# Optimization experiments

Hardware: AMD Instinct MI355X
Metric: run time of the kernel (lower is better)

## Reference

```python
import jax, jax.numpy as jnp
import numpy as np

E = 1024
M = 6
GH = 256
FR = 16  # FiLM bottleneck r = max(16, E//64)


def setup_inputs() -> dict:
    key = jax.random.key(0)
    ks = jax.random.split(key, 32)
    n = lambda k, shape, std=0.02: jax.random.normal(k, shape, dtype=jnp.float32) * std
    inp = {
        "x": jax.random.normal(ks[0], (4, 2048, E), dtype=jnp.float32),
        # gate MLP E->GH->M
        "gw1": n(ks[1], (E, GH)), "gb1": jnp.zeros((GH,), jnp.float32),
        "gw2": n(ks[2], (GH, M)), "gb2": jnp.zeros((M,), jnp.float32),
        "ebias": jnp.zeros((M,), jnp.float32),
        "pm_alpha": jnp.float32(0.5),
        # expert 0: DoubleMLP E->2E->E
        "dfc_w": n(ks[3], (E, 2 * E)), "dfc_b": jnp.zeros((2 * E,), jnp.float32),
        "dproj_w": n(ks[4], (2 * E, E)), "dproj_b": jnp.zeros((E,), jnp.float32),
        # expert 1: SingleMLP E->E->E
        "sfc_w": n(ks[5], (E, E)), "sfc_b": jnp.zeros((E,), jnp.float32),
        "sproj_w": n(ks[6], (E, E)), "sproj_b": jnp.zeros((E,), jnp.float32),
        # expert 2: rank-2 perceptron
        "p2_w": n(ks[7], (2, E)), "p2_v": n(ks[8], (2, E)),
        "p2_alpha": jnp.ones((2,), jnp.float32), "p2_b": jnp.zeros((2,), jnp.float32),
        "p2_bias": jnp.zeros((E,), jnp.float32),
        # expert 3: rank-4 perceptron
        "p4_w": n(ks[9], (4, E)), "p4_v": n(ks[10], (4, E)),
        "p4_alpha": jnp.ones((4,), jnp.float32), "p4_b": jnp.zeros((4,), jnp.float32),
        "p4_bias": jnp.zeros((E,), jnp.float32),
        # expert 4: ReGLU1D
        "rg_u": n(ks[11], (E,)), "rg_a": jnp.ones((E,), jnp.float32),
        "rg_b": jnp.zeros((1,), jnp.float32), "rg_bias": jnp.zeros((E,), jnp.float32),
        # expert 5: FiLM E->FR->2E
        "fl_dw": n(ks[12], (E, FR)), "fl_db": jnp.zeros((FR,), jnp.float32),
        "fl_uw": n(ks[13], (FR, 2 * E)), "fl_ub": jnp.zeros((2 * E,), jnp.float32),
    }
    return inp


def _gelu(x):
    return jax.nn.gelu(x, approximate=False)  # torch nn.GELU default (erf)


def _rank_n(x, w, v, alpha, b, biasvec):
    # y = biasvec + sum_i alpha_i * gelu(<w_i,x> + b_i) * v_i
    s = jnp.einsum("bse,ne->bsn", x, w) + b
    g = _gelu(s)
    return jnp.einsum("bsn,ne->bse", alpha * g, v) + biasvec


def reference(x, gw1, gb1, gw2, gb2, ebias, pm_alpha,
              dfc_w, dfc_b, dproj_w, dproj_b,
              sfc_w, sfc_b, sproj_w, sproj_b,
              p2_w, p2_v, p2_alpha, p2_b, p2_bias,
              p4_w, p4_v, p4_alpha, p4_b, p4_bias,
              rg_u, rg_a, rg_b, rg_bias,
              fl_dw, fl_db, fl_uw, fl_ub):
    # gate logits [B,S,M]; tau=1.0
    gl = _gelu(x @ gw1 + gb1) @ gw2 + gb2 + ebias
    pi = jax.nn.softmax(gl, axis=-1)
    # top_k=1 sparse weights: mask to top-1 then renormalize
    _, topi = jax.lax.top_k(pi, 1)
    mask = jax.nn.one_hot(topi[..., 0], M, dtype=pi.dtype)
    w = pi * mask
    w = w / (jnp.sum(w, axis=-1, keepdims=True) + 1e-9)

    # experts (dropout = identity in eval)
    o0 = _gelu(x @ dfc_w + dfc_b) @ dproj_w + dproj_b            # DoubleMLP
    o1 = _gelu(x @ sfc_w + sfc_b) @ sproj_w + sproj_b            # SingleMLP
    o2 = _rank_n(x, p2_w, p2_v, p2_alpha, p2_b, p2_bias)          # perc2
    o3 = _rank_n(x, p4_w, p4_v, p4_alpha, p4_b, p4_bias)          # perc4
    s = x @ rg_u + rg_b[0]                                        # ReGLU1D
    o4 = jax.nn.sigmoid(s)[..., None] * (x * rg_a) + rg_bias
    t = _gelu(x @ fl_dw + fl_db)                                  # FiLM
    gb = t @ fl_uw + fl_ub
    gamma, beta = jnp.split(gb, 2, axis=-1)
    o5 = gamma * x + beta

    all_out = jnp.stack([o0, o1, o2, o3, o4, o5], axis=-1)        # [B,S,E,M]
    mixed = jnp.sum(all_out * w[..., None, :], axis=-1)
    return pm_alpha * mixed
```

## Files before the change

### kernel.cpp

```cpp
#include <hip/hip_runtime.h>
#include <math.h>


#define E 1024
#define GH 256
#define NEXP 6
#define NTOK 8192

typedef __attribute__((ext_vector_type(8))) short bf16x8;
typedef __attribute__((ext_vector_type(4))) float f32x4;

__device__ __forceinline__ float gelu_erf(float v) {
    return 0.5f * v * (1.0f + erff(v * 0.70710678118654752440f));
}

__device__ __forceinline__ unsigned short f2bf(float f) {
    union { float f; unsigned u; } c; c.f = f;
    unsigned u = c.u;
    u += 0x7fffu + ((u >> 16) & 1u);
    return (unsigned short)(u >> 16);
}

__device__ __forceinline__ float bf2f(unsigned short h) {
    union { unsigned u; float f; } c; c.u = ((unsigned)h) << 16;
    return c.f;
}

__device__ __forceinline__ float dot4(float4 a, float4 b) {
    return a.x * b.x + a.y * b.y + a.z * b.z + a.w * b.w;
}

__device__ __forceinline__ int ldso(int row, int q) {
    return row * 32 + ((q ^ ((row >> 1) & 3)) << 3);
}

__global__ __launch_bounds__(256)
void prep_kernel(const float* __restrict__ x, unsigned short* __restrict__ xh,
                 unsigned short* __restrict__ xl,
                 const float* __restrict__ gw1, unsigned short* __restrict__ w1cat,
                 const float* __restrict__ fl_dw, float* __restrict__ fl_dwT,
                 const float* __restrict__ dfc_w, unsigned short* __restrict__ dfc_wt,
                 const float* __restrict__ dproj_w, unsigned short* __restrict__ dpj_wt,
                 const float* __restrict__ sfc_w, unsigned short* __restrict__ sfc_wt,
                 const float* __restrict__ sproj_w, unsigned short* __restrict__ spj_wt) {
    __shared__ float tile[32][33];
    const int tid = threadIdx.x;
    const int tx = tid & 31, ty = tid >> 5;
    int b = blockIdx.x;
    if (b < 2048) {
        const int n4 = NTOK * E / 4;
        for (int i = b * 256 + tid; i < n4; i += 2048 * 256) {
            float4 v = reinterpret_cast<const float4*>(x)[i];
            ushort4 h, l;
            h.x = f2bf(v.x); l.x = f2bf(v.x - bf2f(h.x));
            h.y = f2bf(v.y); l.y = f2bf(v.y - bf2f(h.y));
            h.z = f2bf(v.z); l.z = f2bf(v.z - bf2f(h.z));
            h.w = f2bf(v.w); l.w = f2bf(v.w - bf2f(h.w));
            reinterpret_cast<ushort4*>(xh)[i] = h;
            reinterpret_cast<ushort4*>(xl)[i] = l;
        }
        return;
    }
    b -= 2048;
    if (b < 256) {
        const int c0 = (b & 7) * 32, r0 = (b >> 3) * 32;
#pragma unroll
        for (int i = 0; i < 4; ++i)
            tile[ty + i * 8][tx] = gw1[(size_t)(r0 + ty + i * 8) * GH + c0 + tx];
        __syncthreads();
#pragma unroll
        for (int i = 0; i < 4; ++i) {
            float v = tile[tx][ty + i * 8];
            unsigned short h = f2bf(v);
            size_t row = (size_t)(c0 + ty + i * 8) * 2048;
            w1cat[row + r0 + tx] = h;
            w1cat[row + 1024 + r0 + tx] = f2bf(v - bf2f(h));
        }
        return;
    }
    b -= 256;
    if (b < 64) {
        int idx = b * 256 + tid;
        int j = idx >> 10, k = idx & (E - 1);
        fl_dwT[idx] = fl_dw[k * 16 + j];
        return;
    }
    b -= 64;
    const float* src; unsigned short* dst; int R, C, nbx;
    if (b < 2048)      { src = dfc_w;   dst = dfc_wt; R = 1024; C = 2048; nbx = 64; }
    else if (b < 4096) { src = dproj_w; dst = dpj_wt; R = 2048; C = 1024; nbx = 32; b -= 2048; }
    else if (b < 5120) { src = sfc_w;   dst = sfc_wt; R = 1024; C = 1024; nbx = 32; b -= 4096; }
    else               { src = sproj_w; dst = spj_wt; R = 1024; C = 1024; nbx = 32; b -= 5120; }
    const int c0 = (b % nbx) * 32, r0 = (b / nbx) * 32;
#pragma unroll
    for (int i = 0; i < 4; ++i)
        tile[ty + i * 8][tx] = src[(size_t)(r0 + ty + i * 8) * C + c0 + tx];
    __syncthreads();
#pragma unroll
    for (int i = 0; i < 4; ++i)
        dst[(size_t)(c0 + ty + i * 8) * R + r0 + tx] = f2bf(tile[tx][ty + i * 8]);
}

__global__ __launch_bounds__(256)
void gate_partial_kernel(const unsigned short* __restrict__ xh,
                         const unsigned short* __restrict__ xl,
                         const unsigned short* __restrict__ w1cat,
                         float* __restrict__ hp0, float* __restrict__ hp1) {
    __shared__ __align__(16) unsigned short As[128 * 32];
    __shared__ __align__(16) unsigned short Bs[64 * 32];
    const int tid = threadIdx.x;
    const int t0 = blockIdx.y * 128, n0 = blockIdx.x * 64, z = blockIdx.z;
    const unsigned short* A = z ? xl : xh;
    float* hp = z ? hp1 : hp0;

    const int lane = tid & 63, wv = tid >> 6;
    const int wm = (wv & 1) * 64, wn = (wv >> 1) * 32;
    const int lm = lane & 15, q = lane >> 4;
    const int r0 = tid >> 2, gsl = tid & 3;
    const int g = gsl ^ ((r0 >> 1) & 3);

    const unsigned short* pa0 = A + (size_t)(t0 + r0) * E + g * 8;
    const unsigned short* pa1 = A + (size_t)(t0 + r0 + 64) * E + g * 8;
    const unsigned short* pb0 = w1cat + (size_t)(n0 + r0) * 2048 + g * 8;

    f32x4 acc[4][2];
#pragma unroll
    for (int s = 0; s < 4; ++s)
#pragma unroll
        for (int t = 0; t < 2; ++t) acc[s][t] = (f32x4){0.f, 0.f, 0.f, 0.f};

    bf16x8 ra0 = *(const bf16x8*)(pa0);
    bf16x8 ra1 = *(const bf16x8*)(pa1);
    bf16x8 rb0 = *(const bf16x8*)(pb0);
    *(bf16x8*)&As[r0 * 32 + gsl * 8] = ra0;
    *(bf16x8*)&As[(r0 + 64) * 32 + gsl * 8] = ra1;
    *(bf16x8*)&Bs[r0 * 32 + gsl * 8] = rb0;

    int k0 = 0;
    while (true) {
        __syncthreads();
        const int kn = k0 + 32;
        if (kn < 2048) {
            ra0 = *(const bf16x8*)(pa0 + (kn & 1023));
            ra1 = *(const bf16x8*)(pa1 + (kn & 1023));
            rb0 = *(const bf16x8*)(pb0 + kn);
        }
        bf16x8 af[4], bf[2];
#pragma unroll
        for (int s = 0; s < 4; ++s) af[s] = *(const bf16x8*)&As[ldso(wm + s * 16 + lm, q)];
#pragma unroll
        for (int t = 0; t < 2; ++t) bf[t] = *(const bf16x8*)&Bs[ldso(wn + t * 16 + lm, q)];
#pragma unroll
        for (int s = 0; s < 4; ++s)
#pragma unroll
            for (int t = 0; t < 2; ++t)
                acc[s][t] = __builtin_amdgcn_mfma_f32_16x16x32_bf16(af[s], bf[t], acc[s][t], 0, 0, 0);
        if (kn >= 2048) break;
        __syncthreads();
        *(bf16x8*)&As[r0 * 32 + gsl * 8] = ra0;
        *(bf16x8*)&As[(r0 + 64) * 32 + gsl * 8] = ra1;
        *(bf16x8*)&Bs[r0 * 32 + gsl * 8] = rb0;
        k0 = kn;
    }
#pragma unroll
    for (int s = 0; s < 4; ++s)
#pragma unroll
        for (int t = 0; t < 2; ++t)
#pragma unroll
            for (int rg = 0; rg < 4; ++rg) {
                int rl = wm + s * 16 + q * 4 + rg;
                int c  = wn + t * 16 + lm;
                hp[(size_t)(t0 + rl) * GH + n0 + c] = acc[s][t][rg];
            }
}

__global__ __launch_bounds__(256)
void gate_finalize_kernel(const float* __restrict__ hp0, const float* __restrict__ hp1,
                          const float* __restrict__ gb1, const float* __restrict__ gw2,
                          const float* __restrict__ gb2, const float* __restrict__ ebias,
                          const float* __restrict__ pm_alpha,
                          float* __restrict__ scale, int* __restrict__ counts,
                          int* __restrict__ tlist, int* __restrict__ eid) {
    __shared__ float hs[32][264];
    __shared__ float g2s[GH * NEXP];
    __shared__ int tokexp[32];
    const int tid = threadIdx.x;
    const int t0 = blockIdx.x * 32;
    for (int i = tid; i < GH * NEXP; i += 256) g2s[i] = gw2[i];
#pragma unroll
    for (int i = 0; i < 8; ++i) {
        int f4 = i * 256 + tid;
        int row = f4 >> 6, c4 = (f4 & 63) * 4;
        size_t base = (size_t)(t0 + row) * GH + c4;
        float4 a = *reinterpret_cast<const float4*>(&hp0[base]);
        float4 b = *reinterpret_cast<const float4*>(&hp1[base]);
        float4 o;
        o.x = gelu_erf(a.x + b.x + gb1[c4 + 0]);
        o.y = gelu_erf(a.y + b.y + gb1[c4 + 1]);
        o.z = gelu_erf(a.z + b.z + gb1[c4 + 2]);
        o.w = gelu_erf(a.w + b.w + gb1[c4 + 3]);
        *reinterpret_cast<float4*>(&hs[row][c4]) = o;
    }
    __syncthreads();
    const int t = tid >> 3, j = tid & 7;
    float p[NEXP] = {0.f, 0.f, 0.f, 0.f, 0.f, 0.f};
#pragma unroll 8
    for (int kk = 0; kk < 32; ++kk) {
        int k = j + kk * 8;
        float hv = hs[t][k];
        const float* gr = &g2s[k * NEXP];
#pragma unroll
        for (int m = 0; m < NEXP; ++m) p[m] += hv * gr[m];
    }
#pragma unroll
    for (int m = 0; m < NEXP; ++m) {
        p[m] += __shfl_xor(p[m], 4, 64);
        p[m] += __shfl_xor(p[m], 2, 64);
        p[m] += __shfl_xor(p[m], 1, 64);
    }
    if (j == 0) {
        float L[NEXP];
#pragma unroll
        for (int m = 0; m < NEXP; ++m) L[m] = p[m] + gb2[m] + ebias[m];
        float mx = L[0]; int am = 0;
#pragma unroll
        for (int m = 1; m < NEXP; ++m) { if (L[m] > mx) { mx = L[m]; am = m; } }
        float S = 0.f;
#pragma unroll
        for (int m = 0; m < NEXP; ++m) S += expf(L[m] - mx);
        float pt = 1.f / S;
        scale[t0 + t] = pm_alpha[0] * (pt / (pt + 1e-9f));
        eid[t0 + t] = am;
        tokexp[t] = am;
    }
    __syncthreads();
    if (tid < NEXP) {
        const int e = tid;
        int cnt = 0;
#pragma unroll
        for (int i = 0; i < 32; ++i) cnt += (tokexp[i] == e);
        if (cnt) {
            int base = atomicAdd(&counts[e], cnt);
            int pos = 0;
#pragma unroll
            for (int i = 0; i < 32; ++i)
                if (tokexp[i] == e) tlist[e * NTOK + base + (pos++)] = t0 + i;
        }
    }
}

__global__ __launch_bounds__(256)
void moe_gemm1_kernel(const unsigned short* __restrict__ xh,
                      const unsigned short* __restrict__ B0, const unsigned short* __restrict__ B1,
                      const float* __restrict__ bias0, const float* __restrict__ bias1,
                      const int* __restrict__ counts, const int* __restrict__ tlist,
                      unsigned short* __restrict__ H0, unsigned short* __restrict__ H1) {
    const int z = blockIdx.z;
    const int N = z ? 1024 : 2048;
    const int K = E;
    const int cnt = counts[z];
    const int i0 = blockIdx.y * 64;
    const int n0 = blockIdx.x * 64;
    if (i0 >= cnt || n0 >= N) return;
    const unsigned short* Bz = z ? B1 : B0;
    const float* bias = z ? bias1 : bias0;

    __shared__ __align__(16) unsigned short As[64 * 32];
    __shared__ __align__(16) unsigned short Bs[64 * 32];
    __shared__ int toks[64];
    const int tid = threadIdx.x;
    if (tid < 64) toks[tid] = tlist[z * NTOK + min(i0 + tid, cnt - 1)];
    __syncthreads();

    const int lane = tid & 63, wv = tid >> 6;
    const int wm = (wv & 1) * 32, wn = (wv >> 1) * 32;
    const int lm = lane & 15, q = lane >> 4;
    const int r0 = tid >> 2, gsl = tid & 3;
    const int g = gsl ^ ((r0 >> 1) & 3);

    const unsigned short* pa = xh + (size_t)toks[r0] * K + g * 8;
    const unsigned short* pb = Bz + (size_t)(n0 + r0) * K + g * 8;

    f32x4 acc[2][2];
#pragma unroll
    for (int s = 0; s < 2; ++s)
#pragma unroll
        for (int t = 0; t < 2; ++t) acc[s][t] = (f32x4){0.f, 0.f, 0.f, 0.f};

    bf16x8 ra = *(const bf16x8*)(pa);
    bf16x8 rb = *(const bf16x8*)(pb);
    *(bf16x8*)&As[r0 * 32 + gsl * 8] = ra;
    *(bf16x8*)&Bs[r0 * 32 + gsl * 8] = rb;

    int k0 = 0;
    while (true) {
        __syncthreads();
        const int kn = k0 + 32;
        if (kn < K) {
            ra = *(const bf16x8*)(pa + kn);
            rb = *(const bf16x8*)(pb + kn);
        }
        bf16x8 af[2], bf[2];
#pragma unroll
        for (int s = 0; s < 2; ++s) af[s] = *(const bf16x8*)&As[ldso(wm + s * 16 + lm, q)];
#pragma unroll
        for (int t = 0; t < 2; ++t) bf[t] = *(const bf16x8*)&Bs[ldso(wn + t * 16 + lm, q)];
#pragma unroll
        for (int s = 0; s < 2; ++s)
#pragma unroll
            for (int t = 0; t < 2; ++t)
                acc[s][t] = __builtin_amdgcn_mfma_f32_16x16x32_bf16(af[s], bf[t], acc[s][t], 0, 0, 0);
        if (kn >= K) break;
        __syncthreads();
        *(bf16x8*)&As[r0 * 32 + gsl * 8] = ra;
        *(bf16x8*)&Bs[r0 * 32 + gsl * 8] = rb;
        k0 = kn;
    }
    unsigned short* Hz = z ? H1 : H0;
#pragma unroll
    for (int s = 0; s < 2; ++s)
#pragma unroll
        for (int t = 0; t < 2; ++t)
#pragma unroll
            for (int rg = 0; rg < 4; ++rg) {
                int rl = wm + s * 16 + q * 4 + rg;
                int gc = n0 + wn + t * 16 + lm;
                float v = acc[s][t][rg] + bias[gc];
                Hz[(size_t)(i0 + rl) * N + gc] = f2bf(gelu_erf(v));
            }
}

__global__ __launch_bounds__(256)
void gemm2_cheap_kernel(const unsigned short* __restrict__ h1, const unsigned short* __restrict__ h2,
                        const unsigned short* __restrict__ dpj, const unsigned short* __restrict__ spj,
                        const float* __restrict__ dproj_b, const float* __restrict__ sproj_b,
                        const int* __restrict__ counts, const int* __restrict__ tlist,
                        const float* __restrict__ scale,
                        const float* __restrict__ x, const int* __restrict__ eid,
                        const float* __restrict__ p2_w, const float* __restrict__ p2_v,
                        const float* __restrict__ p2_alpha, const float* __restrict__ p2_b,
                        const float* __restrict__ p2_bias,
                        const float* __restrict__ p4_w, const float* __restrict__ p4_v,
                        const float* __restrict__ p4_alpha, const float* __restrict__ p4_b,
                        const float* __restrict__ p4_bias,
                        const float* __restrict__ rg_u, const float* __restrict__ rg_a,
                        const float* __restrict__ rg_b, const float* __restrict__ rg_bias,
                        const float* __restrict__ fl_dwT, const float* __restrict__ fl_db,
                        const float* __restrict__ fl_uw, const float* __restrict__ fl_ub,
                        float* __restrict__ out) {
    __shared__ __align__(16) char smem[64 * 32 * 2 * 2 + 64 * 4];
    const int tid = threadIdx.x;
    const int bb = blockIdx.x;

    if (bb < 1024) {
        const int z = bb >> 9;
        const int r = bb & 511;
        const int n0 = (r & 15) * 64;
        const int i0 = (r >> 4) * 64;
        const int K = z ? 1024 : 2048;
        const int cnt = counts[z];
        if (i0 >= cnt) return;
        const int rows = min(64, cnt - i0);
        const unsigned short* Az = z ? h2 : h1;
        const unsigned short* Bz = z ? spj : dpj;
        const float* bias = z ? sproj_b : dproj_b;

        unsigned short* As = (unsigned short*)smem;
        unsigned short* Bs = As + 64 * 32;
        int* toks = (int*)(Bs + 64 * 32);
        if (tid < 64) toks[tid] = tlist[z * NTOK + min(i0 + tid, cnt - 1)];
        __syncthreads();

        const int lane = tid & 63, wv = tid >> 6;
        const int wm = (wv & 1) * 32, wn = (wv >> 1) * 32;
        const int lm = lane & 15, q = lane >> 4;
        const int r0 = tid >> 2, gsl = tid & 3;
        const int g = gsl ^ ((r0 >> 1) & 3);

        const unsigned short* pa = Az + (size_t)(i0 + r0) * K + g * 8;
        const unsigned short* pb = Bz + (size_t)(n0 + r0) * K + g * 8;

        f32x4 acc[2][2];
#pragma unroll
        for (int s = 0; s < 2; ++s)
#pragma unroll
            for (int t = 0; t < 2; ++t) acc[s][t] = (f32x4){0.f, 0.f, 0.f, 0.f};

        bf16x8 ra = *(const bf16x8*)(pa);
        bf16x8 rb = *(const bf16x8*)(pb);
        *(bf16x8*)&As[r0 * 32 + gsl * 8] = ra;
        *(bf16x8*)&Bs[r0 * 32 + gsl * 8] = rb;

        int k0 = 0;
        while (true) {
            __syncthreads();
            const int kn = k0 + 32;
            if (kn < K) {
                ra = *(const bf16x8*)(pa + kn);
                rb = *(const bf16x8*)(pb + kn);
            }
            bf16x8 af[2], bf[2];
#pragma unroll
            for (int s = 0; s < 2; ++s) af[s] = *(const bf16x8*)&As[ldso(wm + s * 16 + lm, q)];
#pragma unroll
            for (int t = 0; t < 2; ++t) bf[t] = *(const bf16x8*)&Bs[ldso(wn + t * 16 + lm, q)];
#pragma unroll
            for (int s = 0; s < 2; ++s)
#pragma unroll
                for (int t = 0; t < 2; ++t)
                    acc[s][t] = __builtin_amdgcn_mfma_f32_16x16x32_bf16(af[s], bf[t], acc[s][t], 0, 0, 0);
            if (kn >= K) break;
            __syncthreads();
            *(bf16x8*)&As[r0 * 32 + gsl * 8] = ra;
            *(bf16x8*)&Bs[r0 * 32 + gsl * 8] = rb;
            k0 = kn;
        }
#pragma unroll
        for (int s = 0; s < 2; ++s)
#pragma unroll
            for (int t = 0; t < 2; ++t)
#pragma unroll
                for (int rg = 0; rg < 4; ++rg) {
                    int rl = wm + s * 16 + q * 4 + rg;
                    if (rl < rows) {
                        int gc = n0 + wn + t * 16 + lm;
                        int tok = toks[rl];
                        out[(size_t)tok * E + gc] = scale[tok] * (acc[s][t][rg] + bias[gc]);
                    }
                }
        return;
    }

    const int tok = bb - 1024;
    const int e = eid[tok];
    if (e < 2) return;
    float* red = (float*)smem;
    float* gs  = red + 64;
    const int k4 = tid * 4;
    const float4 xv = *reinterpret_cast<const float4*>(&x[(size_t)tok * E + k4]);
    const float sc = scale[tok];
    const int lane = tid & 63, wid = tid >> 6;
    float4 o;

    if (e == 2 || e == 3) {
        const int n = (e == 2) ? 2 : 4;
        const float* w    = (e == 2) ? p2_w : p4_w;
        const float* v    = (e == 2) ? p2_v : p4_v;
        const float* al   = (e == 2) ? p2_alpha : p4_alpha;
        const float* b    = (e == 2) ? p2_b : p4_b;
        const float* bias = (e == 2) ? p2_bias : p4_bias;
        for (int j = 0; j < n; ++j) {
            float val = dot4(xv, *reinterpret_cast<const float4*>(&w[j * E + k4]));
            for (int off = 32; off > 0; off >>= 1) val += __shfl_down(val, off, 64);
            if (lane == 0) red[j * 4 + wid] = val;
        }
        __syncthreads();
        if (tid < n) {
            float s = red[tid * 4] + red[tid * 4 + 1] + red[tid * 4 + 2] + red[tid * 4 + 3] + b[tid];
            gs[tid] = al[tid] * gelu_erf(s);
        }
        __syncthreads();
        o = *reinterpret_cast<const float4*>(&bias[k4]);
        for (int j = 0; j < n; ++j) {
            float4 vv = *reinterpret_cast<const float4*>(&v[j * E + k4]);
            float gj = gs[j];
            o.x += gj * vv.x; o.y += gj * vv.y; o.z += gj * vv.z; o.w += gj * vv.w;
        }
    } else if (e == 4) {
        float val = dot4(xv, *reinterpret_cast<const float4*>(&rg_u[k4]));
        for (int off = 32; off > 0; off >>= 1) val += __shfl_down(val, off, 64);
        if (lane == 0) red[wid] = val;
        __syncthreads();
        float s = red[0] + red[1] + red[2] + red[3] + rg_b[0];
        float sg = 1.f / (1.f + expf(-s));
        float4 av = *reinterpret_cast<const float4*>(&rg_a[k4]);
        float4 bv = *reinterpret_cast<const float4*>(&rg_bias[k4]);
        o.x = sg * xv.x * av.x + bv.x;
        o.y = sg * xv.y * av.y + bv.y;
        o.z = sg * xv.z * av.z + bv.z;
        o.w = sg * xv.w * av.w + bv.w;
    } else {
#pragma unroll
        for (int j = 0; j < 16; ++j) {
            float val = dot4(xv, *reinterpret_cast<const float4*>(&fl_dwT[j * E + k4]));
            for (int off = 32; off > 0; off >>= 1) val += __shfl_down(val, off, 64);
            if (lane == 0) red[j * 4 + wid] = val;
        }
        __syncthreads();
        if (tid < 16)
            gs[tid] = gelu_erf(red[tid * 4] + red[tid * 4 + 1] + red[tid * 4 + 2] + red[tid * 4 + 3] + fl_db[tid]);
        __syncthreads();
        float4 ga = *reinterpret_cast<const float4*>(&fl_ub[k4]);
        float4 be = *reinterpret_cast<const float4*>(&fl_ub[E + k4]);
#pragma unroll
        for (int j = 0; j < 16; ++j) {
            float tj = gs[j];
            float4 ug = *reinterpret_cast<const float4*>(&fl_uw[(size_t)j * 2 * E + k4]);
            float4 ub = *reinterpret_cast<const float4*>(&fl_uw[(size_t)j * 2 * E + E + k4]);
            ga.x += tj * ug.x; ga.y += tj * ug.y; ga.z += tj * ug.z; ga.w += tj * ug.w;
            be.x += tj * ub.x; be.y += tj * ub.y; be.z += tj * ub.z; be.w += tj * ub.w;
        }
        o.x = ga.x * xv.x + be.x;
        o.y = ga.y * xv.y + be.y;
        o.z = ga.z * xv.z + be.z;
        o.w = ga.w * xv.w + be.w;
    }
    o.x *= sc; o.y *= sc; o.z *= sc; o.w *= sc;
    *reinterpret_cast<float4*>(&out[(size_t)tok * E + k4]) = o;
}

extern "C" void kernel_launch(void* const* d_in, const int* in_sizes, int n_in,
                              void* d_out, int out_size, void* d_ws, size_t ws_size,
                              hipStream_t stream) {
    const float* x        = (const float*)d_in[0];
    const float* gw1      = (const float*)d_in[1];
    const float* gb1      = (const float*)d_in[2];
    const float* gw2      = (const float*)d_in[3];
    const float* gb2      = (const float*)d_in[4];
    const float* ebias    = (const float*)d_in[5];
    const float* pm_alpha = (const float*)d_in[6];
    const float* dfc_w    = (const float*)d_in[7];
    const float* dfc_b    = (const float*)d_in[8];
    const float* dproj_w  = (const float*)d_in[9];
    const float* dproj_b  = (const float*)d_in[10];
    const float* sfc_w    = (const float*)d_in[11];
    const float* sfc_b    = (const float*)d_in[12];
    const float* sproj_w  = (const float*)d_in[13];
    const float* sproj_b  = (const float*)d_in[14];
    const float* p2_w     = (const float*)d_in[15];
    const float* p2_v     = (const float*)d_in[16];
    const float* p2_alpha = (const float*)d_in[17];
    const float* p2_b     = (const float*)d_in[18];
    const float* p2_bias  = (const float*)d_in[19];
    const float* p4_w     = (const float*)d_in[20];
    const float* p4_v     = (const float*)d_in[21];
    const float* p4_alpha = (const float*)d_in[22];
    const float* p4_b     = (const float*)d_in[23];
    const float* p4_bias  = (const float*)d_in[24];
    const float* rg_u     = (const float*)d_in[25];
    const float* rg_a     = (const float*)d_in[26];
    const float* rg_b     = (const float*)d_in[27];
    const float* rg_bias  = (const float*)d_in[28];
    const float* fl_dw    = (const float*)d_in[29];
    const float* fl_db    = (const float*)d_in[30];
    const float* fl_uw    = (const float*)d_in[31];
    const float* fl_ub    = (const float*)d_in[32];
    float* out = (float*)d_out;

    char* ws = (char*)d_ws;
    size_t off = 0;
    int*            counts = (int*)(ws + off);            off += 256;
    float*          scale  = (float*)(ws + off);          off += (size_t)NTOK * 4;
    int*            tlist  = (int*)(ws + off);            off += (size_t)NEXP * NTOK * 4;
    int*            eid    = (int*)(ws + off);            off += (size_t)NTOK * 4;
    float*          fl_dwT = (float*)(ws + off);          off += (size_t)16 * E * 4;
    unsigned short* w1cat  = (unsigned short*)(ws + off); off += (size_t)GH * 2048 * 2;
    unsigned short* dfc_wt = (unsigned short*)(ws + off); off += (size_t)2048 * 1024 * 2;
    unsigned short* dpj_wt = (unsigned short*)(ws + off); off += (size_t)1024 * 2048 * 2;
    unsigned short* sfc_wt = (unsigned short*)(ws + off); off += (size_t)1024 * 1024 * 2;
    unsigned short* spj_wt = (unsigned short*)(ws + off); off += (size_t)1024 * 1024 * 2;
    unsigned short* x_hi   = (unsigned short*)(ws + off); off += (size_t)NTOK * E * 2;
    char* U = ws + off;
    unsigned short* x_lo = (unsigned short*)U;
    float*          hp0  = (float*)(U + (size_t)16 * 1024 * 1024);
    float*          hp1  = (float*)(U + (size_t)24 * 1024 * 1024);
    unsigned short* h1   = (unsigned short*)U;
    unsigned short* h2   = (unsigned short*)(U + (size_t)16 * 1024 * 1024);

    hipMemsetAsync(counts, 0, 256, stream);
    prep_kernel<<<8512, 256, 0, stream>>>(x, x_hi, x_lo, gw1, w1cat, fl_dw, fl_dwT,
                                          dfc_w, dfc_wt, dproj_w, dpj_wt,
                                          sfc_w, sfc_wt, sproj_w, spj_wt);
    gate_partial_kernel<<<dim3(GH / 64, NTOK / 128, 2), 256, 0, stream>>>(x_hi, x_lo, w1cat, hp0, hp1);
    gate_finalize_kernel<<<NTOK / 32, 256, 0, stream>>>(hp0, hp1, gb1, gw2, gb2, ebias,
                                                        pm_alpha, scale, counts, tlist, eid);
    moe_gemm1_kernel<<<dim3(32, 32, 2), 256, 0, stream>>>(
        x_hi, dfc_wt, sfc_wt, dfc_b, sfc_b, counts, tlist, h1, h2);
    gemm2_cheap_kernel<<<1024 + NTOK, 256, 0, stream>>>(
        h1, h2, dpj_wt, spj_wt, dproj_b, sproj_b, counts, tlist, scale,
        x, eid,
        p2_w, p2_v, p2_alpha, p2_b, p2_bias,
        p4_w, p4_v, p4_alpha, p4_b, p4_bias,
        rg_u, rg_a, rg_b, rg_bias,
        fl_dwT, fl_db, fl_uw, fl_ub, out);
    (void)in_sizes; (void)n_in; (void)out_size; (void)ws_size;
}
```

Before: 297.9 us.

## Merge all stages into one cooperative persistent kernel with grid syncs

Replaces the memset and five separate kernel launches with a single cooperative persistent kernel. Phases are separated by grid.sync(), and each phase handles work units in a grid-stride loop. The gate GEMM is co-scheduled with the weight transposes so the two can overlap. This removes launch gaps and tail effects between stages, at the cost of grid-wide barriers, a grid capped at 1024 blocks, and register pressure from the merged code under launch_bounds(256,4).

```diff
diff --git a/kernel.cpp b/kernel.cpp
--- a/kernel.cpp
+++ b/kernel.cpp
@@ -1,5 +1,8 @@
 #include <hip/hip_runtime.h>
+#include <hip/hip_cooperative_groups.h>
 #include <math.h>
+
+namespace cg = cooperative_groups;
 
 
 #define E 1024
@@ -34,554 +37,512 @@
     return row * 32 + ((q ^ ((row >> 1) & 3)) << 3);
 }
 
-__global__ __launch_bounds__(256)
-void prep_kernel(const float* __restrict__ x, unsigned short* __restrict__ xh,
-                 unsigned short* __restrict__ xl,
-                 const float* __restrict__ gw1, unsigned short* __restrict__ w1cat,
-                 const float* __restrict__ fl_dw, float* __restrict__ fl_dwT,
-                 const float* __restrict__ dfc_w, unsigned short* __restrict__ dfc_wt,
-                 const float* __restrict__ dproj_w, unsigned short* __restrict__ dpj_wt,
-                 const float* __restrict__ sfc_w, unsigned short* __restrict__ sfc_wt,
-                 const float* __restrict__ sproj_w, unsigned short* __restrict__ spj_wt) {
-    __shared__ float tile[32][33];
-    const int tid = threadIdx.x;
-    const int tx = tid & 31, ty = tid >> 5;
-    int b = blockIdx.x;
-    if (b < 2048) {
-        const int n4 = NTOK * E / 4;
-        for (int i = b * 256 + tid; i < n4; i += 2048 * 256) {
-            float4 v = reinterpret_cast<const float4*>(x)[i];
-            ushort4 h, l;
-            h.x = f2bf(v.x); l.x = f2bf(v.x - bf2f(h.x));
-            h.y = f2bf(v.y); l.y = f2bf(v.y - bf2f(h.y));
-            h.z = f2bf(v.z); l.z = f2bf(v.z - bf2f(h.z));
-            h.w = f2bf(v.w); l.w = f2bf(v.w - bf2f(h.w));
-            reinterpret_cast<ushort4*>(xh)[i] = h;
-            reinterpret_cast<ushort4*>(xl)[i] = l;
-        }
-        return;
-    }
-    b -= 2048;
-    if (b < 256) {
-        const int c0 = (b & 7) * 32, r0 = (b >> 3) * 32;
-#pragma unroll
-        for (int i = 0; i < 4; ++i)
-            tile[ty + i * 8][tx] = gw1[(size_t)(r0 + ty + i * 8) * GH + c0 + tx];
-        __syncthreads();
-#pragma unroll
-        for (int i = 0; i < 4; ++i) {
-            float v = tile[tx][ty + i * 8];
-            unsigned short h = f2bf(v);
-            size_t row = (size_t)(c0 + ty + i * 8) * 2048;
-            w1cat[row + r0 + tx] = h;
-            w1cat[row + 1024 + r0 + tx] = f2bf(v - bf2f(h));
-        }
-        return;
-    }
-    b -= 256;
-    if (b < 64) {
-        int idx = b * 256 + tid;
-        int j = idx >> 10, k = idx & (E - 1);
-        fl_dwT[idx] = fl_dw[k * 16 + j];
-        return;
-    }
-    b -= 64;
-    const float* src; unsigned short* dst; int R, C, nbx;
-    if (b < 2048)      { src = dfc_w;   dst = dfc_wt; R = 1024; C = 2048; nbx = 64; }
-    else if (b < 4096) { src = dproj_w; dst = dpj_wt; R = 2048; C = 1024; nbx = 32; b -= 2048; }
-    else if (b < 5120) { src = sfc_w;   dst = sfc_wt; R = 1024; C = 1024; nbx = 32; b -= 4096; }
-    else               { src = sproj_w; dst = spj_wt; R = 1024; C = 1024; nbx = 32; b -= 5120; }
-    const int c0 = (b % nbx) * 32, r0 = (b / nbx) * 32;
-#pragma unroll
-    for (int i = 0; i < 4; ++i)
-        tile[ty + i * 8][tx] = src[(size_t)(r0 + ty + i * 8) * C + c0 + tx];
-    __syncthreads();
-#pragma unroll
-    for (int i = 0; i < 4; ++i)
-        dst[(size_t)(c0 + ty + i * 8) * R + r0 + tx] = f2bf(tile[tx][ty + i * 8]);
-}
-
-__global__ __launch_bounds__(256)
-void gate_partial_kernel(const unsigned short* __restrict__ xh,
-                         const unsigned short* __restrict__ xl,
-                         const unsigned short* __restrict__ w1cat,
-                         float* __restrict__ hp0, float* __restrict__ hp1) {
-    __shared__ __align__(16) unsigned short As[128 * 32];
-    __shared__ __align__(16) unsigned short Bs[64 * 32];
-    const int tid = threadIdx.x;
-    const int t0 = blockIdx.y * 128, n0 = blockIdx.x * 64, z = blockIdx.z;
-    const unsigned short* A = z ? xl : xh;
-    float* hp = z ? hp1 : hp0;
-
-    const int lane = tid & 63, wv = tid >> 6;
-    const int wm = (wv & 1) * 64, wn = (wv >> 1) * 32;
-    const int lm = lane & 15, q = lane >> 4;
-    const int r0 = tid >> 2, gsl = tid & 3;
-    const int g = gsl ^ ((r0 >> 1) & 3);
-
-    const unsigned short* pa0 = A + (size_t)(t0 + r0) * E + g * 8;
-    const unsigned short* pa1 = A + (size_t)(t0 + r0 + 64) * E + g * 8;
-    const unsigned short* pb0 = w1cat + (size_t)(n0 + r0) * 2048 + g * 8;
-
-    f32x4 acc[4][2];
-#pragma unroll
-    for (int s = 0; s < 4; ++s)
-#pragma unroll
-        for (int t = 0; t < 2; ++t) acc[s][t] = (f32x4){0.f, 0.f, 0.f, 0.f};
-
-    bf16x8 ra0 = *(const bf16x8*)(pa0);
-    bf16x8 ra1 = *(const bf16x8*)(pa1);
-    bf16x8 rb0 = *(const bf16x8*)(pb0);
-    *(bf16x8*)&As[r0 * 32 + gsl * 8] = ra0;
-    *(bf16x8*)&As[(r0 + 64) * 32 + gsl * 8] = ra1;
-    *(bf16x8*)&Bs[r0 * 32 + gsl * 8] = rb0;
-
-    int k0 = 0;
-    while (true) {
-        __syncthreads();
-        const int kn = k0 + 32;
-        if (kn < 2048) {
-            ra0 = *(const bf16x8*)(pa0 + (kn & 1023));
-            ra1 = *(const bf16x8*)(pa1 + (kn & 1023));
-            rb0 = *(const bf16x8*)(pb0 + kn);
-        }
-        bf16x8 af[4], bf[2];
-#pragma unroll
-        for (int s = 0; s < 4; ++s) af[s] = *(const bf16x8*)&As[ldso(wm + s * 16 + lm, q)];
-#pragma unroll
-        for (int t = 0; t < 2; ++t) bf[t] = *(const bf16x8*)&Bs[ldso(wn + t * 16 + lm, q)];
-#pragma unroll
-        for (int s = 0; s < 4; ++s)
-#pragma unroll
-            for (int t = 0; t < 2; ++t)
-                acc[s][t] = __builtin_amdgcn_mfma_f32_16x16x32_bf16(af[s], bf[t], acc[s][t], 0, 0, 0);
-        if (kn >= 2048) break;
-        __syncthreads();
-        *(bf16x8*)&As[r0 * 32 + gsl * 8] = ra0;
-        *(bf16x8*)&As[(r0 + 64) * 32 + gsl * 8] = ra1;
-        *(bf16x8*)&Bs[r0 * 32 + gsl * 8] = rb0;
-        k0 = kn;
-    }
-#pragma unroll
-    for (int s = 0; s < 4; ++s)
-#pragma unroll
-        for (int t = 0; t < 2; ++t)
-#pragma unroll
-            for (int rg = 0; rg < 4; ++rg) {
-                int rl = wm + s * 16 + q * 4 + rg;
-                int c  = wn + t * 16 + lm;
-                hp[(size_t)(t0 + rl) * GH + n0 + c] = acc[s][t][rg];
+struct MoeParams {
+    const float *x, *gw1, *gb1, *gw2, *gb2, *ebias, *pm_alpha;
+    const float *dfc_w, *dfc_b, *dproj_w, *dproj_b;
+    const float *sfc_w, *sfc_b, *sproj_w, *sproj_b;
+    const float *p2_w, *p2_v, *p2_alpha, *p2_b, *p2_bias;
+    const float *p4_w, *p4_v, *p4_alpha, *p4_b, *p4_bias;
+    const float *rg_u, *rg_a, *rg_b, *rg_bias;
+    const float *fl_dw, *fl_db, *fl_uw, *fl_ub;
+    float* out;
+    int* counts; float* scale; int* tlist; int* eid; float* fl_dwT;
+    unsigned short *w1cat, *dfc_wt, *dpj_wt, *sfc_wt, *spj_wt, *x_hi, *x_lo;
+    float *hp0, *hp1;
+    unsigned short *h1, *h2;
+};
+
+__global__ __launch_bounds__(256, 4)
+void moe_mega_kernel(MoeParams P) {
+    cg::grid_group grid = cg::this_grid();
+    __shared__ __align__(16) char smem[12544];
+    const int tid  = threadIdx.x;
+    const int nb   = gridDim.x;
+    const int lane = tid & 63, wvi = tid >> 6;
+
+    if (blockIdx.x == 0 && tid < 64) P.counts[tid] = 0;
+    {
+        float (*tile)[33] = (float (*)[33])smem;
+        const int tx = tid & 31, ty = tid >> 5;
+        for (int u = blockIdx.x; u < 2304; u += nb) {
+            if (u < 2048) {
+                const int base = u * 1024 + tid;
+#pragma unroll
+                for (int ii = 0; ii < 4; ++ii) {
+                    const int i = base + ii * 256;
+                    float4 v = reinterpret_cast<const float4*>(P.x)[i];
+                    ushort4 h, l;
+                    h.x = f2bf(v.x); l.x = f2bf(v.x - bf2f(h.x));
+                    h.y = f2bf(v.y); l.y = f2bf(v.y - bf2f(h.y));
+                    h.z = f2bf(v.z); l.z = f2bf(v.z - bf2f(h.z));
+                    h.w = f2bf(v.w); l.w = f2bf(v.w - bf2f(h.w));
+                    reinterpret_cast<ushort4*>(P.x_hi)[i] = h;
+                    reinterpret_cast<ushort4*>(P.x_lo)[i] = l;
+                }
+            } else {
+                const int b = u - 2048;
+                const int c0 = (b & 7) * 32, r0 = (b >> 3) * 32;
+                __syncthreads();
+#pragma unroll
+                for (int i = 0; i < 4; ++i)
+                    tile[ty + i * 8][tx] = P.gw1[(size_t)(r0 + ty + i * 8) * GH + c0 + tx];
+                __syncthreads();
+#pragma unroll
+                for (int i = 0; i < 4; ++i) {
+                    float v = tile[tx][ty + i * 8];
+                    unsigned short h = f2bf(v);
+                    size_t row = (size_t)(c0 + ty + i * 8) * 2048;
+                    P.w1cat[row + r0 + tx] = h;
+                    P.w1cat[row + 1024 + r0 + tx] = f2bf(v - bf2f(h));
+                }
             }
-}
-
-__global__ __launch_bounds__(256)
-void gate_finalize_kernel(const float* __restrict__ hp0, const float* __restrict__ hp1,
-                          const float* __restrict__ gb1, const float* __restrict__ gw2,
-                          const float* __restrict__ gb2, const float* __restrict__ ebias,
-                          const float* __restrict__ pm_alpha,
-                          float* __restrict__ scale, int* __restrict__ counts,
-                          int* __restrict__ tlist, int* __restrict__ eid) {
-    __shared__ float hs[32][264];
-    __shared__ float g2s[GH * NEXP];
-    __shared__ int tokexp[32];
-    const int tid = threadIdx.x;
-    const int t0 = blockIdx.x * 32;
-    for (int i = tid; i < GH * NEXP; i += 256) g2s[i] = gw2[i];
-#pragma unroll
-    for (int i = 0; i < 8; ++i) {
-        int f4 = i * 256 + tid;
-        int row = f4 >> 6, c4 = (f4 & 63) * 4;
-        size_t base = (size_t)(t0 + row) * GH + c4;
-        float4 a = *reinterpret_cast<const float4*>(&hp0[base]);
-        float4 b = *reinterpret_cast<const float4*>(&hp1[base]);
-        float4 o;
-        o.x = gelu_erf(a.x + b.x + gb1[c4 + 0]);
-        o.y = gelu_erf(a.y + b.y + gb1[c4 + 1]);
-        o.z = gelu_erf(a.z + b.z + gb1[c4 + 2]);
-        o.w = gelu_erf(a.w + b.w + gb1[c4 + 3]);
-        *reinterpret_cast<float4*>(&hs[row][c4]) = o;
-    }
-    __syncthreads();
-    const int t = tid >> 3, j = tid & 7;
-    float p[NEXP] = {0.f, 0.f, 0.f, 0.f, 0.f, 0.f};
-#pragma unroll 8
-    for (int kk = 0; kk < 32; ++kk) {
-        int k = j + kk * 8;
-        float hv = hs[t][k];
-        const float* gr = &g2s[k * NEXP];
-#pragma unroll
-        for (int m = 0; m < NEXP; ++m) p[m] += hv * gr[m];
-    }
-#pragma unroll
-    for (int m = 0; m < NEXP; ++m) {
-        p[m] += __shfl_xor(p[m], 4, 64);
-        p[m] += __shfl_xor(p[m], 2, 64);
-        p[m] += __shfl_xor(p[m], 1, 64);
-    }
-    if (j == 0) {
-        float L[NEXP];
-#pragma unroll
-        for (int m = 0; m < NEXP; ++m) L[m] = p[m] + gb2[m] + ebias[m];
-        float mx = L[0]; int am = 0;
-#pragma unroll
-        for (int m = 1; m < NEXP; ++m) { if (L[m] > mx) { mx = L[m]; am = m; } }
-        float S = 0.f;
-#pragma unroll
-        for (int m = 0; m < NEXP; ++m) S += expf(L[m] - mx);
-        float pt = 1.f / S;
-        scale[t0 + t] = pm_alpha[0] * (pt / (pt + 1e-9f));
-        eid[t0 + t] = am;
-        tokexp[t] = am;
-    }
-    __syncthreads();
-    if (tid < NEXP) {
-        const int e = tid;
-        int cnt = 0;
-#pragma unroll
-        for (int i = 0; i < 32; ++i) cnt += (tokexp[i] == e);
-        if (cnt) {
-            int base = atomicAdd(&counts[e], cnt);
-            int pos = 0;
-#pragma unroll
-            for (int i = 0; i < 32; ++i)
-                if (tokexp[i] == e) tlist[e * NTOK + base + (pos++)] = t0 + i;
         }
     }
-}
-
-__global__ __launch_bounds__(256)
-void moe_gemm1_kernel(const unsigned short* __restrict__ xh,
-                      const unsigned short* __restrict__ B0, const unsigned short* __restrict__ B1,
-                      const float* __restrict__ bias0, const float* __restrict__ bias1,
-                      const int* __restrict__ counts, const int* __restrict__ tlist,
-                      unsigned short* __restrict__ H0, unsigned short* __restrict__ H1) {
-    const int z = blockIdx.z;
-    const int N = z ? 1024 : 2048;
-    const int K = E;
-    const int cnt = counts[z];
-    const int i0 = blockIdx.y * 64;
-    const int n0 = blockIdx.x * 64;
-    if (i0 >= cnt || n0 >= N) return;
-    const unsigned short* Bz = z ? B1 : B0;
-    const float* bias = z ? bias1 : bias0;
-
-    __shared__ __align__(16) unsigned short As[64 * 32];
-    __shared__ __align__(16) unsigned short Bs[64 * 32];
-    __shared__ int toks[64];
-    const int tid = threadIdx.x;
-    if (tid < 64) toks[tid] = tlist[z * NTOK + min(i0 + tid, cnt - 1)];
-    __syncthreads();
-
-    const int lane = tid & 63, wv = tid >> 6;
-    const int wm = (wv & 1) * 32, wn = (wv >> 1) * 32;
-    const int lm = lane & 15, q = lane >> 4;
-    const int r0 = tid >> 2, gsl = tid & 3;
-    const int g = gsl ^ ((r0 >> 1) & 3);
-
-    const unsigned short* pa = xh + (size_t)toks[r0] * K + g * 8;
-    const unsigned short* pb = Bz + (size_t)(n0 + r0) * K + g * 8;
-
-    f32x4 acc[2][2];
-#pragma unroll
-    for (int s = 0; s < 2; ++s)
-#pragma unroll
-        for (int t = 0; t < 2; ++t) acc[s][t] = (f32x4){0.f, 0.f, 0.f, 0.f};
-
-    bf16x8 ra = *(const bf16x8*)(pa);
-    bf16x8 rb = *(const bf16x8*)(pb);
-    *(bf16x8*)&As[r0 * 32 + gsl * 8] = ra;
-    *(bf16x8*)&Bs[r0 * 32 + gsl * 8] = rb;
-
-    int k0 = 0;
-    while (true) {
-        __syncthreads();
-        const int kn = k0 + 32;
-        if (kn < K) {
-            ra = *(const bf16x8*)(pa + kn);
-            rb = *(const bf16x8*)(pb + kn);
+    grid.sync();
+
+    {
+        const int wm = (wvi & 1) * 64, wn = (wvi >> 1) * 32;
+        const int lm = lane & 15, q = lane >> 4;
+        const int r0t = tid >> 2, gsl = tid & 3;
+        const int g = gsl ^ ((r0t >> 1) & 3);
+        unsigned short* As = (unsigned short*)smem;
+        unsigned short* Bs = As + 128 * 32;
+        float (*tile)[33] = (float (*)[33])smem;
+        const int tx = tid & 31, ty = tid >> 5;
+        for (int u = blockIdx.x; u < 6720; u += nb) {
+            if (u < 512) {
+                const int z = u >> 8, r = u & 255;
+                const int n0 = (r & 3) * 64, t0 = (r >> 2) * 128;
+                const unsigned short* A = z ? P.x_lo : P.x_hi;
+                float* hp = z ? P.hp1 : P.hp0;
+                const unsigned short* pa0 = A + (size_t)(t0 + r0t) * E + g * 8;
+                const unsigned short* pa1 = A + (size_t)(t0 + r0t + 64) * E + g * 8;
+                const unsigned short* pb0 = P.w1cat + (size_t)(n0 + r0t) * 2048 + g * 8;
+                f32x4 acc[4][2];
+#pragma unroll
+                for (int s = 0; s < 4; ++s)
+#pragma unroll
+                    for (int t = 0; t < 2; ++t) acc[s][t] = (f32x4){0.f, 0.f, 0.f, 0.f};
+                bf16x8 ra0 = *(const bf16x8*)(pa0);
+                bf16x8 ra1 = *(const bf16x8*)(pa1);
+                bf16x8 rb0 = *(const bf16x8*)(pb0);
+                __syncthreads();
+                *(bf16x8*)&As[r0t * 32 + gsl * 8] = ra0;
+                *(bf16x8*)&As[(r0t + 64) * 32 + gsl * 8] = ra1;
+                *(bf16x8*)&Bs[r0t * 32 + gsl * 8] = rb0;
+                int k0 = 0;
+                while (true) {
+                    __syncthreads();
+                    const int kn = k0 + 32;
+                    if (kn < 2048) {
+                        ra0 = *(const bf16x8*)(pa0 + (kn & 1023));
+                        ra1 = *(const bf16x8*)(pa1 + (kn & 1023));
+                        rb0 = *(const bf16x8*)(pb0 + kn);
+                    }
+                    bf16x8 af[4], bf[2];
+#pragma unroll
+                    for (int s = 0; s < 4; ++s) af[s] = *(const bf16x8*)&As[ldso(wm + s * 16 + lm, q)];
+#pragma unroll
+                    for (int t = 0; t < 2; ++t) bf[t] = *(const bf16x8*)&Bs[ldso(wn + t * 16 + lm, q)];
+#pragma unroll
+                    for (int s = 0; s < 4; ++s)
+#pragma unroll
+                        for (int t = 0; t < 2; ++t)
+                            acc[s][t] = __builtin_amdgcn_mfma_f32_16x16x32_bf16(af[s], bf[t], acc[s][t], 0, 0, 0);
+                    if (kn >= 2048) break;
+                    __syncthreads();
+                    *(bf16x8*)&As[r0t * 32 + gsl * 8] = ra0;
+                    *(bf16x8*)&As[(r0t + 64) * 32 + gsl * 8] = ra1;
+                    *(bf16x8*)&Bs[r0t * 32 + gsl * 8] = rb0;
+                    k0 = kn;
+                }
+#pragma unroll
+                for (int s = 0; s < 4; ++s)
+#pragma unroll
+                    for (int t = 0; t < 2; ++t)
+#pragma unroll
+                        for (int rg = 0; rg < 4; ++rg) {
+                            int rl = wm + s * 16 + q * 4 + rg;
+                            int c  = wn + t * 16 + lm;
+                            hp[(size_t)(t0 + rl) * GH + n0 + c] = acc[s][t][rg];
+                        }
+            } else {
+                int b = u - 512;
+                if (b >= 6144) {
+                    int idx = (b - 6144) * 256 + tid;
+                    P.fl_dwT[idx] = P.fl_dw[(idx & (E - 1)) * 16 + (idx >> 10)];
+                    continue;
+                }
+                const float* src; unsigned short* dst; int C, R, nbx;
+                if (b < 2048)      { src = P.dfc_w;   dst = P.dfc_wt; R = 1024; C = 2048; nbx = 64; }
+                else if (b < 4096) { src = P.dproj_w; dst = P.dpj_wt; R = 2048; C = 1024; nbx = 32; b -= 2048; }
+                else if (b < 5120) { src = P.sfc_w;   dst = P.sfc_wt; R = 1024; C = 1024; nbx = 32; b -= 4096; }
+                else               { src = P.sproj_w; dst = P.spj_wt; R = 1024; C = 1024; nbx = 32; b -= 5120; }
+                const int c0 = (b % nbx) * 32, r0 = (b / nbx) * 32;
+                __syncthreads();
+#pragma unroll
+                for (int i = 0; i < 4; ++i)
+                    tile[ty + i * 8][tx] = src[(size_t)(r0 + ty + i * 8) * C + c0 + tx];
+                __syncthreads();
+#pragma unroll
+                for (int i = 0; i < 4; ++i)
+                    dst[(size_t)(c0 + ty + i * 8) * R + r0 + tx] = f2bf(tile[tx][ty + i * 8]);
+            }
         }
-        bf16x8 af[2], bf[2];
-#pragma unroll
-        for (int s = 0; s < 2; ++s) af[s] = *(const bf16x8*)&As[ldso(wm + s * 16 + lm, q)];
-#pragma unroll
-        for (int t = 0; t < 2; ++t) bf[t] = *(const bf16x8*)&Bs[ldso(wn + t * 16 + lm, q)];
-#pragma unroll
-        for (int s = 0; s < 2; ++s)
-#pragma unroll
-            for (int t = 0; t < 2; ++t)
-                acc[s][t] = __builtin_amdgcn_mfma_f32_16x16x32_bf16(af[s], bf[t], acc[s][t], 0, 0, 0);
-        if (kn >= K) break;
-        __syncthreads();
-        *(bf16x8*)&As[r0 * 32 + gsl * 8] = ra;
-        *(bf16x8*)&Bs[r0 * 32 + gsl * 8] = rb;
-        k0 = kn;
     }
-    unsigned short* Hz = z ? H1 : H0;
-#pragma unroll
-    for (int s = 0; s < 2; ++s)
-#pragma unroll
-        for (int t = 0; t < 2; ++t)
-#pragma unroll
-            for (int rg = 0; rg < 4; ++rg) {
-                int rl = wm + s * 16 + q * 4 + rg;
-                int gc = n0 + wn + t * 16 + lm;
-                float v = acc[s][t][rg] + bias[gc];
-                Hz[(size_t)(i0 + rl) * N + gc] = f2bf(gelu_erf(v));
+    grid.sync();
+
+    {
+        float* g2s  = (float*)smem;
+        int* tokexp = (int*)(smem + 6144);
+        for (int u = blockIdx.x; u < 256; u += nb) {
+            __syncthreads();
+            for (int i = tid; i < GH * NEXP; i += 256) g2s[i] = P.gw2[i];
+            __syncthreads();
+            const int t0 = u * 32;
+            const int tkg = tid >> 5, j = tid & 31;
+#pragma unroll
+            for (int rep = 0; rep < 4; ++rep) {
+                const int t = t0 + tkg * 4 + rep;
+                float p[NEXP] = {0.f, 0.f, 0.f, 0.f, 0.f, 0.f};
+                const size_t base = (size_t)t * GH;
+#pragma unroll
+                for (int kk = 0; kk < 8; ++kk) {
+                    const int k = j + kk * 32;
+                    float hv = gelu_erf(P.hp0[base + k] + P.hp1[base + k] + P.gb1[k]);
+                    const float* gr = &g2s[k * NEXP];
+#pragma unroll
+                    for (int m = 0; m < NEXP; ++m) p[m] += hv * gr[m];
+                }
+#pragma unroll
+                for (int m = 0; m < NEXP; ++m) {
+                    p[m] += __shfl_xor(p[m], 16, 64);
+                    p[m] += __shfl_xor(p[m], 8, 64);
+                    p[m] += __shfl_xor(p[m], 4, 64);
+                    p[m] += __shfl_xor(p[m], 2, 64);
+                    p[m] += __shfl_xor(p[m], 1, 64);
+                }
+                if (j == 0) {
+                    float L[NEXP];
+#pragma unroll
+                    for (int m = 0; m < NEXP; ++m) L[m] = p[m] + P.gb2[m] + P.ebias[m];
+                    float mx = L[0]; int am = 0;
+#pragma unroll
+                    for (int m = 1; m < NEXP; ++m) { if (L[m] > mx) { mx = L[m]; am = m; } }
+                    float S = 0.f;
+#pragma unroll
+                    for (int m = 0; m < NEXP; ++m) S += expf(L[m] - mx);
+                    float pt = 1.f / S;
+                    P.scale[t] = P.pm_alpha[0] * (pt / (pt + 1e-9f));
+                    P.eid[t] = am;
+                    tokexp[tkg * 4 + rep] = am;
+                }
             }
-}
-
-__global__ __launch_bounds__(256)
-void gemm2_cheap_kernel(const unsigned short* __restrict__ h1, const unsigned short* __restrict__ h2,
-                        const unsigned short* __restrict__ dpj, const unsigned short* __restrict__ spj,
-                        const float* __restrict__ dproj_b, const float* __restrict__ sproj_b,
-                        const int* __restrict__ counts, const int* __restrict__ tlist,
-                        const float* __restrict__ scale,
-                        const float* __restrict__ x, const int* __restrict__ eid,
-                        const float* __restrict__ p2_w, const float* __restrict__ p2_v,
-                        const float* __restrict__ p2_alpha, const float* __restrict__ p2_b,
-                        const float* __restrict__ p2_bias,
-                        const float* __restrict__ p4_w, const float* __restrict__ p4_v,
-                        const float* __restrict__ p4_alpha, const float* __restrict__ p4_b,
-                        const float* __restrict__ p4_bias,
-                        const float* __restrict__ rg_u, const float* __restrict__ rg_a,
-                        const float* __restrict__ rg_b, const float* __restrict__ rg_bias,
-                        const float* __restrict__ fl_dwT, const float* __restrict__ fl_db,
-                        const float* __restrict__ fl_uw, const float* __restrict__ fl_ub,
-                        float* __restrict__ out) {
-    __shared__ __align__(16) char smem[64 * 32 * 2 * 2 + 64 * 4];
-    const int tid = threadIdx.x;
-    const int bb = blockIdx.x;
-
-    if (bb < 1024) {
-        const int z = bb >> 9;
-        const int r = bb & 511;
-        const int n0 = (r & 15) * 64;
-        const int i0 = (r >> 4) * 64;
-        const int K = z ? 1024 : 2048;
-        const int cnt = counts[z];
-        if (i0 >= cnt) return;
-        const int rows = min(64, cnt - i0);
-        const unsigned short* Az = z ? h2 : h1;
-        const unsigned short* Bz = z ? spj : dpj;
-        const float* bias = z ? sproj_b : dproj_b;
-
+            __syncthreads();
+            if (tid < NEXP) {
+                int cnt = 0;
+#pragma unroll
+                for (int i = 0; i < 32; ++i) cnt += (tokexp[i] == tid);
+                if (cnt) {
+                    int bbase = atomicAdd(&P.counts[tid], cnt);
+                    int pos = 0;
+#pragma unroll
+                    for (int i = 0; i < 32; ++i)
+                        if (tokexp[i] == tid) P.tlist[tid * NTOK + bbase + (pos++)] = t0 + i;
+                }
+            }
+        }
+    }
+    grid.sync();
+
+    {
+        const int wm = (wvi & 1) * 32, wn = (wvi >> 1) * 32;
+        const int lm = lane & 15, q = lane >> 4;
+        const int r0t = tid >> 2, gsl = tid & 3;
+        const int g = gsl ^ ((r0t >> 1) & 3);
         unsigned short* As = (unsigned short*)smem;
         unsigned short* Bs = As + 64 * 32;
         int* toks = (int*)(Bs + 64 * 32);
-        if (tid < 64) toks[tid] = tlist[z * NTOK + min(i0 + tid, cnt - 1)];
-        __syncthreads();
-
-        const int lane = tid & 63, wv = tid >> 6;
-        const int wm = (wv & 1) * 32, wn = (wv >> 1) * 32;
+        for (int u = blockIdx.x; u < 1536; u += nb) {
+            int z, n0, i0;
+            if (u < 1024) { z = 0; n0 = (u & 31) * 64; i0 = (u >> 5) * 64; }
+            else { int v = u - 1024; z = 1; n0 = (v & 15) * 64; i0 = (v >> 4) * 64; }
+            const int cnt = P.counts[z];
+            if (i0 >= cnt) continue;
+            const int N = z ? 1024 : 2048;
+            const unsigned short* Bz = z ? P.sfc_wt : P.dfc_wt;
+            const float* bias = z ? P.sfc_b : P.dfc_b;
+            unsigned short* Hz = z ? P.h2 : P.h1;
+            __syncthreads();
+            if (tid < 64) toks[tid] = P.tlist[z * NTOK + min(i0 + tid, cnt - 1)];
+            __syncthreads();
+            const unsigned short* pa = P.x_hi + (size_t)toks[r0t] * E + g * 8;
+            const unsigned short* pb = Bz + (size_t)(n0 + r0t) * E + g * 8;
+            f32x4 acc[2][2];
+#pragma unroll
+            for (int s = 0; s < 2; ++s)
+#pragma unroll
+                for (int t = 0; t < 2; ++t) acc[s][t] = (f32x4){0.f, 0.f, 0.f, 0.f};
+            bf16x8 ra = *(const bf16x8*)(pa);
+            bf16x8 rb = *(const bf16x8*)(pb);
+            *(bf16x8*)&As[r0t * 32 + gsl * 8] = ra;
+            *(bf16x8*)&Bs[r0t * 32 + gsl * 8] = rb;
+            int k0 = 0;
+            while (true) {
+                __syncthreads();
+                const int kn = k0 + 32;
+                if (kn < E) {
+                    ra = *(const bf16x8*)(pa + kn);
+                    rb = *(const bf16x8*)(pb + kn);
+                }
+                bf16x8 af[2], bf[2];
+#pragma unroll
+                for (int s = 0; s < 2; ++s) af[s] = *(const bf16x8*)&As[ldso(wm + s * 16 + lm, q)];
+#pragma unroll
+                for (int t = 0; t < 2; ++t) bf[t] = *(const bf16x8*)&Bs[ldso(wn + t * 16 + lm, q)];
+#pragma unroll
+                for (int s = 0; s < 2; ++s)
+#pragma unroll
+                    for (int t = 0; t < 2; ++t)
+                        acc[s][t] = __builtin_amdgcn_mfma_f32_16x16x32_bf16(af[s], bf[t], acc[s][t], 0, 0, 0);
+                if (kn >= E) break;
+                __syncthreads();
+                *(bf16x8*)&As[r0t * 32 + gsl * 8] = ra;
+                *(bf16x8*)&Bs[r0t * 32 + gsl * 8] = rb;
+                k0 = kn;
+            }
+#pragma unroll
+            for (int s = 0; s < 2; ++s)
+#pragma unroll
+                for (int t = 0; t < 2; ++t)
+#pragma unroll
+                    for (int rg = 0; rg < 4; ++rg) {
+                        int rl = wm + s * 16 + q * 4 + rg;
+                        int gc = n0 + wn + t * 16 + lm;
+                        float v = acc[s][t][rg] + bias[gc];
+                        Hz[(size_t)(i0 + rl) * N + gc] = f2bf(gelu_erf(v));
+                    }
+        }
+    }
+    grid.sync();
+
+    {
+        const int wm = (wvi & 1) * 32, wn = (wvi >> 1) * 32;
         const int lm = lane & 15, q = lane >> 4;
-        const int r0 = tid >> 2, gsl = tid & 3;
-        const int g = gsl ^ ((r0 >> 1) & 3);
-
-        const unsigned short* pa = Az + (size_t)(i0 + r0) * K + g * 8;
-        const unsigned short* pb = Bz + (size_t)(n0 + r0) * K + g * 8;
-
-        f32x4 acc[2][2];
-#pragma unroll
-        for (int s = 0; s < 2; ++s)
-#pragma unroll
-            for (int t = 0; t < 2; ++t) acc[s][t] = (f32x4){0.f, 0.f, 0.f, 0.f};
-
-        bf16x8 ra = *(const bf16x8*)(pa);
-        bf16x8 rb = *(const bf16x8*)(pb);
-        *(bf16x8*)&As[r0 * 32 + gsl * 8] = ra;
-        *(bf16x8*)&Bs[r0 * 32 + gsl * 8] = rb;
-
-        int k0 = 0;
-        while (true) {
-            __syncthreads();
-            const int kn = k0 + 32;
-            if (kn < K) {
-                ra = *(const bf16x8*)(pa + kn);
-                rb = *(const bf16x8*)(pb + kn);
+        const int r0t = tid >> 2, gsl = tid & 3;
+        const int g = gsl ^ ((r0t >> 1) & 3);
+        unsigned short* As = (unsigned short*)smem;
+        unsigned short* Bs = As + 64 * 32;
+        int* toks = (int*)(Bs + 64 * 32);
+        float* red = (float*)smem;
+        float* gs  = red + 64;
+        for (int u = blockIdx.x; u < 1024 + NTOK; u += nb) {
+            if (u < 1024) {
+                const int z = u >> 9, r = u & 511;
+                const int n0 = (r & 15) * 64, i0 = (r >> 4) * 64;
+                const int cnt = P.counts[z];
+                if (i0 >= cnt) continue;
+                const int rows = min(64, cnt - i0);
+                const int K = z ? 1024 : 2048;
+                const unsigned short* Az = z ? P.h2 : P.h1;
+                const unsigned short* Bz = z ? P.spj_wt : P.dpj_wt;
+                const float* bias = z ? P.sproj_b : P.dproj_b;
+                __syncthreads();
+                if (tid < 64) toks[tid] = P.tlist[z * NTOK + min(i0 + tid, cnt - 1)];
+                __syncthreads();
+                const unsigned short* pa = Az + (size_t)(i0 + r0t) * K + g * 8;
+                const unsigned short* pb = Bz + (size_t)(n0 + r0t) * K + g * 8;
+                f32x4 acc[2][2];
+#pragma unroll
+                for (int s = 0; s < 2; ++s)
+#pragma unroll
+                    for (int t = 0; t < 2; ++t) acc[s][t] = (f32x4){0.f, 0.f, 0.f, 0.f};
+                bf16x8 ra = *(const bf16x8*)(pa);
+                bf16x8 rb = *(const bf16x8*)(pb);
+                *(bf16x8*)&As[r0t * 32 + gsl * 8] = ra;
+                *(bf16x8*)&Bs[r0t * 32 + gsl * 8] = rb;
+                int k0 = 0;
+                while (true) {
+                    __syncthreads();
+                    const int kn = k0 + 32;
+                    if (kn < K) {
+                        ra = *(const bf16x8*)(pa + kn);
+                        rb = *(const bf16x8*)(pb + kn);
+                    }
+                    bf16x8 af[2], bf[2];
+#pragma unroll
+                    for (int s = 0; s < 2; ++s) af[s] = *(const bf16x8*)&As[ldso(wm + s * 16 + lm, q)];
+#pragma unroll
+                    for (int t = 0; t < 2; ++t) bf[t] = *(const bf16x8*)&Bs[ldso(wn + t * 16 + lm, q)];
+#pragma unroll
+                    for (int s = 0; s < 2; ++s)
+#pragma unroll
+                        for (int t = 0; t < 2; ++t)
+                            acc[s][t] = __builtin_amdgcn_mfma_f32_16x16x32_bf16(af[s], bf[t], acc[s][t], 0, 0, 0);
+                    if (kn >= K) break;
+                    __syncthreads();
+                    *(bf16x8*)&As[r0t * 32 + gsl * 8] = ra;
+                    *(bf16x8*)&Bs[r0t * 32 + gsl * 8] = rb;
+                    k0 = kn;
+                }
+#pragma unroll
+                for (int s = 0; s < 2; ++s)
+#pragma unroll
+                    for (int t = 0; t < 2; ++t)
+#pragma unroll
+                        for (int rg = 0; rg < 4; ++rg) {
+                            int rl = wm + s * 16 + q * 4 + rg;
+                            if (rl < rows) {
+                                int gc = n0 + wn + t * 16 + lm;
+                                int tok = toks[rl];
+                                P.out[(size_t)tok * E + gc] = P.scale[tok] * (acc[s][t][rg] + bias[gc]);
+                            }
+                        }
+            } else {
+                const int tok = u - 1024;
+                const int e = P.eid[tok];
+                if (e < 2) continue;
+                __syncthreads();
+                const int k4 = tid * 4;
+                const float4 xv = *reinterpret_cast<const float4*>(&P.x[(size_t)tok * E + k4]);
+                const float sc = P.scale[tok];
+                const int wid = tid >> 6;
+                float4 o;
+                if (e == 2 || e == 3) {
+                    const int n = (e == 2) ? 2 : 4;
+                    const float* w    = (e == 2) ? P.p2_w : P.p4_w;
+                    const float* v    = (e == 2) ? P.p2_v : P.p4_v;
+                    const float* al   = (e == 2) ? P.p2_alpha : P.p4_alpha;
+                    const float* b    = (e == 2) ? P.p2_b : P.p4_b;
+                    const float* bias = (e == 2) ? P.p2_bias : P.p4_bias;
+                    for (int j = 0; j < n; ++j) {
+                        float val = dot4(xv, *reinterpret_cast<const float4*>(&w[j * E + k4]));
+                        for (int off = 32; off > 0; off >>= 1) val += __shfl_down(val, off, 64);
+                        if (lane == 0) red[j * 4 + wid] = val;
+                    }
+                    __syncthreads();
+                    if (tid < n) {
+                        float s = red[tid * 4] + red[tid * 4 + 1] + red[tid * 4 + 2] + red[tid * 4 + 3] + b[tid];
+                        gs[tid] = al[tid] * gelu_erf(s);
+                    }
+                    __syncthreads();
+                    o = *reinterpret_cast<const float4*>(&bias[k4]);
+                    for (int j = 0; j < n; ++j) {
+                        float4 vv = *reinterpret_cast<const float4*>(&v[j * E + k4]);
+                        float gj = gs[j];
+                        o.x += gj * vv.x; o.y += gj * vv.y; o.z += gj * vv.z; o.w += gj * vv.w;
+                    }
+                } else if (e == 4) {
+                    float val = dot4(xv, *reinterpret_cast<const float4*>(&P.rg_u[k4]));
+                    for (int off = 32; off > 0; off >>= 1) val += __shfl_down(val, off, 64);
+                    if (lane == 0) red[wid] = val;
+                    __syncthreads();
+                    float s = red[0] + red[1] + red[2] + red[3] + P.rg_b[0];
+                    float sg = 1.f / (1.f + expf(-s));
+                    float4 av = *reinterpret_cast<const float4*>(&P.rg_a[k4]);
+                    float4 bv = *reinterpret_cast<const float4*>(&P.rg_bias[k4]);
+                    o.x = sg * xv.x * av.x + bv.x;
+                    o.y = sg * xv.y * av.y + bv.y;
+                    o.z = sg * xv.z * av.z + bv.z;
+                    o.w = sg * xv.w * av.w + bv.w;
+                } else {
+#pragma unroll
+                    for (int j = 0; j < 16; ++j) {
+                        float val = dot4(xv, *reinterpret_cast<const float4*>(&P.fl_dwT[j * E + k4]));
+                        for (int off = 32; off > 0; off >>= 1) val += __shfl_down(val, off, 64);
+                        if (lane == 0) red[j * 4 + wid] = val;
+                    }
+                    __syncthreads();
+                    if (tid < 16)
+                        gs[tid] = gelu_erf(red[tid * 4] + red[tid * 4 + 1] + red[tid * 4 + 2] + red[tid * 4 + 3] + P.fl_db[tid]);
+                    __syncthreads();
+                    float4 ga = *reinterpret_cast<const float4*>(&P.fl_ub[k4]);
+                    float4 be = *reinterpret_cast<const float4*>(&P.fl_ub[E + k4]);
+#pragma unroll
+                    for (int j = 0; j < 16; ++j) {
+                        float tj = gs[j];
+                        float4 ug = *reinterpret_cast<const float4*>(&P.fl_uw[(size_t)j * 2 * E + k4]);
+                        float4 ub = *reinterpret_cast<const float4*>(&P.fl_uw[(size_t)j * 2 * E + E + k4]);
+                        ga.x += tj * ug.x; ga.y += tj * ug.y; ga.z += tj * ug.z; ga.w += tj * ug.w;
+                        be.x += tj * ub.x; be.y += tj * ub.y; be.z += tj * ub.z; be.w += tj * ub.w;
+                    }
+                    o.x = ga.x * xv.x + be.x;
+                    o.y = ga.y * xv.y + be.y;
+                    o.z = ga.z * xv.z + be.z;
+                    o.w = ga.w * xv.w + be.w;
+                }
+                o.x *= sc; o.y *= sc; o.z *= sc; o.w *= sc;
+                *reinterpret_cast<float4*>(&P.out[(size_t)tok * E + k4]) = o;
             }
-            bf16x8 af[2], bf[2];
-#pragma unroll
-            for (int s = 0; s < 2; ++s) af[s] = *(const bf16x8*)&As[ldso(wm + s * 16 + lm, q)];
-#pragma unroll
-            for (int t = 0; t < 2; ++t) bf[t] = *(const bf16x8*)&Bs[ldso(wn + t * 16 + lm, q)];
-#pragma unroll
-            for (int s = 0; s < 2; ++s)
-#pragma unroll
-                for (int t = 0; t < 2; ++t)
-                    acc[s][t] = __builtin_amdgcn_mfma_f32_16x16x32_bf16(af[s], bf[t], acc[s][t], 0, 0, 0);
-            if (kn >= K) break;
-            __syncthreads();
-            *(bf16x8*)&As[r0 * 32 + gsl * 8] = ra;
-            *(bf16x8*)&Bs[r0 * 32 + gsl * 8] = rb;
-            k0 = kn;
         }
-#pragma unroll
-        for (int s = 0; s < 2; ++s)
-#pragma unroll
-            for (int t = 0; t < 2; ++t)
-#pragma unroll
-                for (int rg = 0; rg < 4; ++rg) {
-                    int rl = wm + s * 16 + q * 4 + rg;
-                    if (rl < rows) {
-                        int gc = n0 + wn + t * 16 + lm;
-                        int tok = toks[rl];
-                        out[(size_t)tok * E + gc] = scale[tok] * (acc[s][t][rg] + bias[gc]);
-                    }
-                }
-        return;
     }
-
-    const int tok = bb - 1024;
-    const int e = eid[tok];
-    if (e < 2) return;
-    float* red = (float*)smem;
-    float* gs  = red + 64;
-    const int k4 = tid * 4;
-    const float4 xv = *reinterpret_cast<const float4*>(&x[(size_t)tok * E + k4]);
-    const float sc = scale[tok];
-    const int lane = tid & 63, wid = tid >> 6;
-    float4 o;
-
-    if (e == 2 || e == 3) {
-        const int n = (e == 2) ? 2 : 4;
-        const float* w    = (e == 2) ? p2_w : p4_w;
-        const float* v    = (e == 2) ? p2_v : p4_v;
-        const float* al   = (e == 2) ? p2_alpha : p4_alpha;
-        const float* b    = (e == 2) ? p2_b : p4_b;
-        const float* bias = (e == 2) ? p2_bias : p4_bias;
-        for (int j = 0; j < n; ++j) {
-            float val = dot4(xv, *reinterpret_cast<const float4*>(&w[j * E + k4]));
-            for (int off = 32; off > 0; off >>= 1) val += __shfl_down(val, off, 64);
-            if (lane == 0) red[j * 4 + wid] = val;
-        }
-        __syncthreads();
-        if (tid < n) {
-            float s = red[tid * 4] + red[tid * 4 + 1] + red[tid * 4 + 2] + red[tid * 4 + 3] + b[tid];
-            gs[tid] = al[tid] * gelu_erf(s);
-        }
-        __syncthreads();
-        o = *reinterpret_cast<const float4*>(&bias[k4]);
-        for (int j = 0; j < n; ++j) {
-            float4 vv = *reinterpret_cast<const float4*>(&v[j * E + k4]);
-            float gj = gs[j];
-            o.x += gj * vv.x; o.y += gj * vv.y; o.z += gj * vv.z; o.w += gj * vv.w;
-        }
-    } else if (e == 4) {
-        float val = dot4(xv, *reinterpret_cast<const float4*>(&rg_u[k4]));
-        for (int off = 32; off > 0; off >>= 1) val += __shfl_down(val, off, 64);
-        if (lane == 0) red[wid] = val;
-        __syncthreads();
-        float s = red[0] + red[1] + red[2] + red[3] + rg_b[0];
-        float sg = 1.f / (1.f + expf(-s));
-        float4 av = *reinterpret_cast<const float4*>(&rg_a[k4]);
-        float4 bv = *reinterpret_cast<const float4*>(&rg_bias[k4]);
-        o.x = sg * xv.x * av.x + bv.x;
-        o.y = sg * xv.y * av.y + bv.y;
-        o.z = sg * xv.z * av.z + bv.z;
-        o.w = sg * xv.w * av.w + bv.w;
-    } else {
-#pragma unroll
-        for (int j = 0; j < 16; ++j) {
-            float val = dot4(xv, *reinterpret_cast<const float4*>(&fl_dwT[j * E + k4]));
-            for (int off = 32; off > 0; off >>= 1) val += __shfl_down(val, off, 64);
-            if (lane == 0) red[j * 4 + wid] = val;
-        }
-        __syncthreads();
-        if (tid < 16)
-            gs[tid] = gelu_erf(red[tid * 4] + red[tid * 4 + 1] + red[tid * 4 + 2] + red[tid * 4 + 3] + fl_db[tid]);
-        __syncthreads();
-        float4 ga = *reinterpret_cast<const float4*>(&fl_ub[k4]);
-        float4 be = *reinterpret_cast<const float4*>(&fl_ub[E + k4]);
-#pragma unroll
-        for (int j = 0; j < 16; ++j) {
-            float tj = gs[j];
-            float4 ug = *reinterpret_cast<const float4*>(&fl_uw[(size_t)j * 2 * E + k4]);
-            float4 ub = *reinterpret_cast<const float4*>(&fl_uw[(size_t)j * 2 * E + E + k4]);
-            ga.x += tj * ug.x; ga.y += tj * ug.y; ga.z += tj * ug.z; ga.w += tj * ug.w;
-            be.x += tj * ub.x; be.y += tj * ub.y; be.z += tj * ub.z; be.w += tj * ub.w;
-        }
-        o.x = ga.x * xv.x + be.x;
-        o.y = ga.y * xv.y + be.y;
-        o.z = ga.z * xv.z + be.z;
-        o.w = ga.w * xv.w + be.w;
-    }
-    o.x *= sc; o.y *= sc; o.z *= sc; o.w *= sc;
-    *reinterpret_cast<float4*>(&out[(size_t)tok * E + k4]) = o;
 }
 
 extern "C" void kernel_launch(void* const* d_in, const int* in_sizes, int n_in,
                               void* d_out, int out_size, void* d_ws, size_t ws_size,
                               hipStream_t stream) {
-    const float* x        = (const float*)d_in[0];
-    const float* gw1      = (const float*)d_in[1];
-    const float* gb1      = (const float*)d_in[2];
-    const float* gw2      = (const float*)d_in[3];
-    const float* gb2      = (const float*)d_in[4];
-    const float* ebias    = (const float*)d_in[5];
-    const float* pm_alpha = (const float*)d_in[6];
-    const float* dfc_w    = (const float*)d_in[7];
-    const float* dfc_b    = (const float*)d_in[8];
-    const float* dproj_w  = (const float*)d_in[9];
-    const float* dproj_b  = (const float*)d_in[10];
-    const float* sfc_w    = (const float*)d_in[11];
-    const float* sfc_b    = (const float*)d_in[12];
-    const float* sproj_w  = (const float*)d_in[13];
-    const float* sproj_b  = (const float*)d_in[14];
-    const float* p2_w     = (const float*)d_in[15];
-    const float* p2_v     = (const float*)d_in[16];
-    const float* p2_alpha = (const float*)d_in[17];
-    const float* p2_b     = (const float*)d_in[18];
-    const float* p2_bias  = (const float*)d_in[19];
-    const float* p4_w     = (const float*)d_in[20];
-    const float* p4_v     = (const float*)d_in[21];
-    const float* p4_alpha = (const float*)d_in[22];
-    const float* p4_b     = (const float*)d_in[23];
-    const float* p4_bias  = (const float*)d_in[24];
-    const float* rg_u     = (const float*)d_in[25];
-    const float* rg_a     = (const float*)d_in[26];
-    const float* rg_b     = (const float*)d_in[27];
-    const float* rg_bias  = (const float*)d_in[28];
-    const float* fl_dw    = (const float*)d_in[29];
-    const float* fl_db    = (const float*)d_in[30];
-    const float* fl_uw    = (const float*)d_in[31];
-    const float* fl_ub    = (const float*)d_in[32];
-    float* out = (float*)d_out;
+    MoeParams P;
+    P.x        = (const float*)d_in[0];
+    P.gw1      = (const float*)d_in[1];
+    P.gb1      = (const float*)d_in[2];
+    P.gw2      = (const float*)d_in[3];
+    P.gb2      = (const float*)d_in[4];
+    P.ebias    = (const float*)d_in[5];
+    P.pm_alpha = (const float*)d_in[6];
+    P.dfc_w    = (const float*)d_in[7];
+    P.dfc_b    = (const float*)d_in[8];
+    P.dproj_w  = (const float*)d_in[9];
+    P.dproj_b  = (const float*)d_in[10];
+    P.sfc_w    = (const float*)d_in[11];
+    P.sfc_b    = (const float*)d_in[12];
+    P.sproj_w  = (const float*)d_in[13];
+    P.sproj_b  = (const float*)d_in[14];
+    P.p2_w     = (const float*)d_in[15];
+    P.p2_v     = (const float*)d_in[16];
+    P.p2_alpha = (const float*)d_in[17];
+    P.p2_b     = (const float*)d_in[18];
+    P.p2_bias  = (const float*)d_in[19];
+    P.p4_w     = (const float*)d_in[20];
+    P.p4_v     = (const float*)d_in[21];
+    P.p4_alpha = (const float*)d_in[22];
+    P.p4_b     = (const float*)d_in[23];
+    P.p4_bias  = (const float*)d_in[24];
+    P.rg_u     = (const float*)d_in[25];
+    P.rg_a     = (const float*)d_in[26];
+    P.rg_b     = (const float*)d_in[27];
+    P.rg_bias  = (const float*)d_in[28];
+    P.fl_dw    = (const float*)d_in[29];
+    P.fl_db    = (const float*)d_in[30];
+    P.fl_uw    = (const float*)d_in[31];
+    P.fl_ub    = (const float*)d_in[32];
+    P.out = (float*)d_out;
 
     char* ws = (char*)d_ws;
     size_t off = 0;
-    int*            counts = (int*)(ws + off);            off += 256;
-    float*          scale  = (float*)(ws + off);          off += (size_t)NTOK * 4;
-    int*            tlist  = (int*)(ws + off);            off += (size_t)NEXP * NTOK * 4;
-    int*            eid    = (int*)(ws + off);            off += (size_t)NTOK * 4;
-    float*          fl_dwT = (float*)(ws + off);          off += (size_t)16 * E * 4;
-    unsigned short* w1cat  = (unsigned short*)(ws + off); off += (size_t)GH * 2048 * 2;
-    unsigned short* dfc_wt = (unsigned short*)(ws + off); off += (size_t)2048 * 1024 * 2;
-    unsigned short* dpj_wt = (unsigned short*)(ws + off); off += (size_t)1024 * 2048 * 2;
-    unsigned short* sfc_wt = (unsigned short*)(ws + off); off += (size_t)1024 * 1024 * 2;
-    unsigned short* spj_wt = (unsigned short*)(ws + off); off += (size_t)1024 * 1024 * 2;
-    unsigned short* x_hi   = (unsigned short*)(ws + off); off += (size_t)NTOK * E * 2;
+    P.counts = (int*)(ws + off);            off += 256;
+    P.scale  = (float*)(ws + off);          off += (size_t)NTOK * 4;
+    P.tlist  = (int*)(ws + off);            off += (size_t)NEXP * NTOK * 4;
+    P.eid    = (int*)(ws + off);            off += (size_t)NTOK * 4;
+    P.fl_dwT = (float*)(ws + off);          off += (size_t)16 * E * 4;
+    P.w1cat  = (unsigned short*)(ws + off); off += (size_t)GH * 2048 * 2;
+    P.dfc_wt = (unsigned short*)(ws + off); off += (size_t)2048 * 1024 * 2;
+    P.dpj_wt = (unsigned short*)(ws + off); off += (size_t)1024 * 2048 * 2;
+    P.sfc_wt = (unsigned short*)(ws + off); off += (size_t)1024 * 1024 * 2;
+    P.spj_wt = (unsigned short*)(ws + off); off += (size_t)1024 * 1024 * 2;
+    P.x_hi   = (unsigned short*)(ws + off); off += (size_t)NTOK * E * 2;
     char* U = ws + off;
-    unsigned short* x_lo = (unsigned short*)U;
-    float*          hp0  = (float*)(U + (size_t)16 * 1024 * 1024);
-    float*          hp1  = (float*)(U + (size_t)24 * 1024 * 1024);
-    unsigned short* h1   = (unsigned short*)U;
-    unsigned short* h2   = (unsigned short*)(U + (size_t)16 * 1024 * 1024);
-
-    hipMemsetAsync(counts, 0, 256, stream);
-    prep_kernel<<<8512, 256, 0, stream>>>(x, x_hi, x_lo, gw1, w1cat, fl_dw, fl_dwT,
-                                          dfc_w, dfc_wt, dproj_w, dpj_wt,
-                                          sfc_w, sfc_wt, sproj_w, spj_wt);
-    gate_partial_kernel<<<dim3(GH / 64, NTOK / 128, 2), 256, 0, stream>>>(x_hi, x_lo, w1cat, hp0, hp1);
-    gate_finalize_kernel<<<NTOK / 32, 256, 0, stream>>>(hp0, hp1, gb1, gw2, gb2, ebias,
-                                                        pm_alpha, scale, counts, tlist, eid);
-    moe_gemm1_kernel<<<dim3(32, 32, 2), 256, 0, stream>>>(
-        x_hi, dfc_wt, sfc_wt, dfc_b, sfc_b, counts, tlist, h1, h2);
-    gemm2_cheap_kernel<<<1024 + NTOK, 256, 0, stream>>>(
-        h1, h2, dpj_wt, spj_wt, dproj_b, sproj_b, counts, tlist, scale,
-        x, eid,
-        p2_w, p2_v, p2_alpha, p2_b, p2_bias,
-        p4_w, p4_v, p4_alpha, p4_b, p4_bias,
-        rg_u, rg_a, rg_b, rg_bias,
-        fl_dwT, fl_db, fl_uw, fl_ub, out);
+    P.x_lo = (unsigned short*)U;
+    P.hp0  = (float*)(U + (size_t)16 * 1024 * 1024);
+    P.hp1  = (float*)(U + (size_t)24 * 1024 * 1024);
+    P.h1   = (unsigned short*)U;
+    P.h2   = (unsigned short*)(U + (size_t)16 * 1024 * 1024);
+
+    int maxb = 0;
+    hipOccupancyMaxActiveBlocksPerMultiprocessor(&maxb, moe_mega_kernel, 256, 0);
+    if (maxb < 1) maxb = 1;
+    unsigned int nblk = (unsigned int)maxb * 256u;
+    if (nblk > 1024u) nblk = 1024u;
+    void* args[] = { (void*)&P };
+    hipLaunchCooperativeKernel(moe_mega_kernel, dim3(nblk), dim3(256), args, 0, stream);
     (void)in_sizes; (void)n_in; (void)out_size; (void)ws_size;
 }
```

Result: slower. 675.0 us (+126.6%).
